# Performance work log

Hardware: AMD Instinct MI355X
Metric: run time of the kernel (lower is better)

The kernel has to match this reference:

```python
import jax, jax.numpy as jnp
import numpy as np

N = 28  # Optics_simulation(28): fixed optical field size


def _pad_kernel_centered(w, n):
    """Zero-pad a [..., k, k] kernel to [..., n, n] centered, then ifftshift so
    that frequency-domain multiplication gives a centered ('same') circular
    convolution, matching the FFT-based 4f optical conv simulation."""
    k = w.shape[-1]
    pad = n - k
    pb = pad // 2
    pa = pad - pb
    cfg = [(0, 0)] * (w.ndim - 2) + [(pb, pa), (pb, pa)]
    wp = jnp.pad(w, cfg)
    return jnp.fft.ifftshift(wp, axes=(-2, -1))


def setup_inputs() -> dict:
    key = jax.random.key(0)
    k1, k2 = jax.random.split(key)
    B, Cin, Cout, K = 256, 256, 256, 3
    x = jax.random.normal(k1, (B, Cin, N, N), dtype=jnp.float32)
    # kaiming_uniform-ish init scale for a [Cout, Cin, K, K] kernel
    bound = 1.0 / np.sqrt(Cin * K * K)
    kernel = jax.random.uniform(k2, (Cout, Cin, K, K), dtype=jnp.float32,
                                minval=-bound, maxval=bound)
    return {"x": x, "kernel": kernel}


def reference(x, kernel):
    # Faithful to the original forward, including its indexing bug: the inner
    # loop always uses input_channel = 0, so every input channel is convolved
    # with kernel[oc, 0]. By linearity of convolution:
    #   out[b, oc] = sum_ic conv(x[b, ic], kernel[oc, 0])
    #             = conv(sum_ic x[b, ic], kernel[oc, 0])
    xs = x.sum(axis=1)                      # [B, N, N]
    w0 = kernel[:, 0]                       # [O, K, K]
    Fw = jnp.fft.fft2(_pad_kernel_centered(w0, N))   # [O, N, N] complex
    Fx = jnp.fft.fft2(xs)                            # [B, N, N] complex
    out = jnp.fft.ifft2(Fx[:, None, :, :] * Fw[None, :, :, :]).real  # [B,O,N,N]
    return out.astype(x.dtype)
```

## Files before the change

kernel.cpp:

```cpp
#include <hip/hip_runtime.h>

#define NDIM 28
#define SPAT 784
#define STRIPS 196
#define NB 256
#define CIN 256
#define COUT 256
#define SCH 4
#define CPC (CIN / SCH)
#define XSC 36

typedef float f4v __attribute__((ext_vector_type(4)));

__global__ __launch_bounds__(256) void k_sum(const float* __restrict__ x,
                                             float* __restrict__ pbuf) {
    int bid = blockIdx.x;
    int b     = bid >> 2;
    int chunk = bid & 3;
    int t = threadIdx.x;
    if (t >= STRIPS) return;

    const float4* xp = (const float4*)x
        + ((size_t)b * CIN + (size_t)chunk * CPC) * STRIPS + t;
    float ax = 0.f, ay = 0.f, az = 0.f, aw = 0.f;
    #pragma unroll 16
    for (int c = 0; c < CPC; ++c) {
        float4 v = xp[c * STRIPS];
        ax += v.x; ay += v.y; az += v.z; aw += v.w;
    }
    ((float4*)pbuf)[((size_t)b * SCH + chunk) * STRIPS + t] = make_float4(ax, ay, az, aw);
}

__global__ __launch_bounds__(256) void k_conv256(const float* __restrict__ pbuf,
                                                 const float* __restrict__ w,
                                                 float* __restrict__ out) {
    __shared__ float xs[30 * XSC];

    int b = blockIdx.x;
    int t = threadIdx.x;

    if (t < STRIPS) {
        const float4* pp = (const float4*)pbuf + (size_t)b * SCH * STRIPS + t;
        float4 a = pp[0];
        #pragma unroll
        for (int c = 1; c < SCH; ++c) {
            float4 v = pp[c * STRIPS];
            a.x += v.x; a.y += v.y; a.z += v.z; a.w += v.w;
        }
        int i = t / 7, q = t % 7;
        *(float4*)&xs[i * XSC + q * 4] = a;
        if (q == 0)
            *(float4*)&xs[i * XSC + 28] = a;
        if (i < 2) {
            *(float4*)&xs[(i + 28) * XSC + q * 4] = a;
            if (q == 0)
                *(float4*)&xs[(i + 28) * XSC + 28] = a;
        }
    }
    __syncthreads();

    if (t >= STRIPS) return;
    int i  = t / 7;
    int js = (t % 7) * 4;

    float W[3][8];
    #pragma unroll
    for (int a = 0; a < 3; ++a) {
        float4 lo = *(const float4*)&xs[(i + a) * XSC + js];
        float4 hi = *(const float4*)&xs[(i + a) * XSC + js + 4];
        W[a][0] = lo.x; W[a][1] = lo.y; W[a][2] = lo.z; W[a][3] = lo.w;
        W[a][4] = hi.x; W[a][5] = hi.y; W[a][6] = hi.z; W[a][7] = hi.w;
    }

    size_t ob = (size_t)b * COUT * SPAT + i * NDIM + js;

    #pragma unroll 4
    for (int cl = 0; cl < 256; ++cl) {
        const float* wp = w + (size_t)cl * (CIN * 9);
        float o0 = 0.f, o1 = 0.f, o2 = 0.f, o3 = 0.f;
        #pragma unroll
        for (int a = 0; a < 3; ++a) {
            #pragma unroll
            for (int c = 0; c < 3; ++c) {
                float fv = wp[8 - 3 * a - c];
                o0 += fv * W[a][0 + c];
                o1 += fv * W[a][1 + c];
                o2 += fv * W[a][2 + c];
                o3 += fv * W[a][3 + c];
            }
        }
        f4v o = {o0, o1, o2, o3};
        __builtin_nontemporal_store(o, (f4v*)(out + ob + (size_t)cl * SPAT));
    }
}

extern "C" void kernel_launch(void* const* d_in, const int* in_sizes, int n_in,
                              void* d_out, int out_size, void* d_ws, size_t ws_size,
                              hipStream_t stream) {
    const float* x = (const float*)d_in[0];
    const float* w = (const float*)d_in[1];
    float* out = (float*)d_out;
    float* pbuf = (float*)d_ws;

    k_sum    <<<NB * SCH, 256, 0, stream>>>(x, pbuf);
    k_conv256<<<NB,       256, 0, stream>>>(pbuf, w, out);
}
```

Before: 74.24 us.

## Transpose conv grid to per-output-channel blocks with double-buffered padded input planes

Splits the conv stage into a combine kernel that writes circularly padded summed planes to workspace, and a conv kernel where each block owns one output channel. That block keeps its 9 filter taps in registers and loops over all 256 batches, double-buffering the padded planes through shared memory. The aim is to stop every block from reloading weights from global memory for each output channel. The cost is an extra kernel launch, a workspace round trip, and a barrier per batch iteration. The nontemporal stores are replaced by plain stores.

Result: slower. 204.6 us (+175.5%).

```diff
diff --git a/kernel.cpp b/kernel.cpp
--- a/kernel.cpp
+++ b/kernel.cpp
@@ -9,6 +9,7 @@
 #define SCH 4
 #define CPC (CIN / SCH)
 #define XSC 36
+#define PLQ 270
 
 typedef float f4v __attribute__((ext_vector_type(4)));
 
@@ -31,66 +32,90 @@
     ((float4*)pbuf)[((size_t)b * SCH + chunk) * STRIPS + t] = make_float4(ax, ay, az, aw);
 }
 
-__global__ __launch_bounds__(256) void k_conv256(const float* __restrict__ pbuf,
-                                                 const float* __restrict__ w,
-                                                 float* __restrict__ out) {
-    __shared__ float xs[30 * XSC];
-
+__global__ __launch_bounds__(256) void k_combine(const float* __restrict__ pbuf,
+                                                 float* __restrict__ xsph) {
     int b = blockIdx.x;
     int t = threadIdx.x;
+    if (t >= STRIPS) return;
 
-    if (t < STRIPS) {
-        const float4* pp = (const float4*)pbuf + (size_t)b * SCH * STRIPS + t;
-        float4 a = pp[0];
-        #pragma unroll
-        for (int c = 1; c < SCH; ++c) {
-            float4 v = pp[c * STRIPS];
-            a.x += v.x; a.y += v.y; a.z += v.z; a.w += v.w;
+    const float4* pp = (const float4*)pbuf + (size_t)b * SCH * STRIPS + t;
+    float4 a = pp[0];
+    #pragma unroll
+    for (int c = 1; c < SCH; ++c) {
+        float4 v = pp[c * STRIPS];
+        a.x += v.x; a.y += v.y; a.z += v.z; a.w += v.w;
+    }
+    int i = t / 7, q = t % 7;
+    float* base = xsph + (size_t)b * (30 * XSC);
+    *(float4*)(base + i * XSC + q * 4) = a;
+    if (q == 0)
+        *(float4*)(base + i * XSC + 28) = a;
+    if (i < 2) {
+        *(float4*)(base + (i + 28) * XSC + q * 4) = a;
+        if (q == 0)
+            *(float4*)(base + (i + 28) * XSC + 28) = a;
+    }
+}
+
+__global__ __launch_bounds__(256) void k_convT(const float* __restrict__ xsph,
+                                               const float* __restrict__ w,
+                                               float* __restrict__ out) {
+    __shared__ float buf[2][30 * XSC];
+
+    const int co = blockIdx.x;
+    const int t  = threadIdx.x;
+
+    const float* wp = w + (size_t)co * (CIN * 9);
+    float f[9];
+    #pragma unroll
+    for (int k = 0; k < 9; ++k) f[k] = wp[8 - k];
+
+    const int i  = t / 7;
+    const int js = (t % 7) * 4;
+    const int r  = t >> 3;
+    const int c4 = t & 7;
+    const f4v* gp = (const f4v*)xsph;
+
+    if (t < 240)
+        *(f4v*)&buf[0][r * XSC + c4 * 4] = gp[0 * PLQ + r * 9 + c4];
+
+    for (int b = 0; b < NB; ++b) {
+        const int cur = b & 1;
+
+        f4v pre;
+        const bool do_pre = (b + 1 < NB) && (t < 240);
+        if (do_pre)
+            pre = gp[(size_t)(b + 1) * PLQ + r * 9 + c4];
+
+        __syncthreads();
+
+        if (do_pre)
+            *(f4v*)&buf[cur ^ 1][r * XSC + c4 * 4] = pre;
+
+        if (t < STRIPS) {
+            float W[3][8];
+            #pragma unroll
+            for (int a = 0; a < 3; ++a) {
+                float4 lo = *(const float4*)&buf[cur][(i + a) * XSC + js];
+                float4 hi = *(const float4*)&buf[cur][(i + a) * XSC + js + 4];
+                W[a][0] = lo.x; W[a][1] = lo.y; W[a][2] = lo.z; W[a][3] = lo.w;
+                W[a][4] = hi.x; W[a][5] = hi.y; W[a][6] = hi.z; W[a][7] = hi.w;
+            }
+            float o0 = 0.f, o1 = 0.f, o2 = 0.f, o3 = 0.f;
+            #pragma unroll
+            for (int a = 0; a < 3; ++a) {
+                #pragma unroll
+                for (int c = 0; c < 3; ++c) {
+                    float fv = f[3 * a + c];
+                    o0 += fv * W[a][0 + c];
+                    o1 += fv * W[a][1 + c];
+                    o2 += fv * W[a][2 + c];
+                    o3 += fv * W[a][3 + c];
+                }
+            }
+            *(float4*)(out + ((size_t)b * COUT + co) * SPAT + i * NDIM + js)
+                = make_float4(o0, o1, o2, o3);
         }
-        int i = t / 7, q = t % 7;
-        *(float4*)&xs[i * XSC + q * 4] = a;
-        if (q == 0)
-            *(float4*)&xs[i * XSC + 28] = a;
-        if (i < 2) {
-            *(float4*)&xs[(i + 28) * XSC + q * 4] = a;
-            if (q == 0)
-                *(float4*)&xs[(i + 28) * XSC + 28] = a;
-        }
-    }
-    __syncthreads();
-
-    if (t >= STRIPS) return;
-    int i  = t / 7;
-    int js = (t % 7) * 4;
-
-    float W[3][8];
-    #pragma unroll
-    for (int a = 0; a < 3; ++a) {
-        float4 lo = *(const float4*)&xs[(i + a) * XSC + js];
-        float4 hi = *(const float4*)&xs[(i + a) * XSC + js + 4];
-        W[a][0] = lo.x; W[a][1] = lo.y; W[a][2] = lo.z; W[a][3] = lo.w;
-        W[a][4] = hi.x; W[a][5] = hi.y; W[a][6] = hi.z; W[a][7] = hi.w;
-    }
-
-    size_t ob = (size_t)b * COUT * SPAT + i * NDIM + js;
-
-    #pragma unroll 4
-    for (int cl = 0; cl < 256; ++cl) {
-        const float* wp = w + (size_t)cl * (CIN * 9);
-        float o0 = 0.f, o1 = 0.f, o2 = 0.f, o3 = 0.f;
-        #pragma unroll
-        for (int a = 0; a < 3; ++a) {
-            #pragma unroll
-            for (int c = 0; c < 3; ++c) {
-                float fv = wp[8 - 3 * a - c];
-                o0 += fv * W[a][0 + c];
-                o1 += fv * W[a][1 + c];
-                o2 += fv * W[a][2 + c];
-                o3 += fv * W[a][3 + c];
-            }
-        }
-        f4v o = {o0, o1, o2, o3};
-        __builtin_nontemporal_store(o, (f4v*)(out + ob + (size_t)cl * SPAT));
     }
 }
 
@@ -100,8 +125,11 @@
     const float* x = (const float*)d_in[0];
     const float* w = (const float*)d_in[1];
     float* out = (float*)d_out;
+
     float* pbuf = (float*)d_ws;
+    float* xsph = pbuf + (size_t)NB * SCH * SPAT;
 
     k_sum    <<<NB * SCH, 256, 0, stream>>>(x, pbuf);
-    k_conv256<<<NB,       256, 0, stream>>>(pbuf, w, out);
+    k_combine<<<NB,       256, 0, stream>>>(pbuf, xsph);
+    k_convT  <<<NB,       256, 0, stream>>>(xsph, w, out);
 }
```
